# Kernel optimization log

Hardware: AMD Instinct MI355X
Metric: run time of the kernel (lower is better)

## Reference

```python
import jax, jax.numpy as jnp
import numpy as np

NODE_DIM = 128
CTX_DIM = 256
OUT_DIM = 256
GRID_SIZE = 4
SPLINE_ORDER = 3
IN_DIM = 3 * NODE_DIM  # subj + obj + transformed context
N_NODES = 100000
N_EDGES = 100000


def make_grid(in_dim, grid_size, spline_order, grid_range=(-1.0, 1.0)):
    h = (grid_range[1] - grid_range[0]) / grid_size
    g = (np.arange(-spline_order, grid_size + spline_order + 1, dtype=np.float32) * h
         + grid_range[0])  # [grid_size + 2*spline_order + 1]
    return jnp.asarray(np.tile(g[None, :], (in_dim, 1)))  # [in, G]


def b_splines(x, grid, spline_order):
    # x: [N, in], grid: [in, G] -> bases: [N, in, grid_size + spline_order]
    xg = x[:, :, None]
    bases = ((xg >= grid[:, :-1]) & (xg < grid[:, 1:])).astype(x.dtype)
    for k in range(1, spline_order + 1):
        left = (xg - grid[:, : -(k + 1)]) / (grid[:, k:-1] - grid[:, : -(k + 1)]) * bases[..., :-1]
        right = (grid[:, k + 1:] - xg) / (grid[:, k + 1:] - grid[:, 1:-k]) * bases[..., 1:]
        bases = left + right
    return bases


def setup_inputs() -> dict:
    key = jax.random.key(0)
    ks = jax.random.split(key, 8)
    n_coef = GRID_SIZE + SPLINE_ORDER
    return {
        "node_embeddings": jax.random.normal(ks[0], (N_NODES, NODE_DIM), jnp.float32),
        "context_embeddings": jax.random.normal(ks[1], (N_EDGES, CTX_DIM), jnp.float32),
        "pair_indices": jax.random.randint(ks[2], (N_EDGES, 2), 0, N_NODES, jnp.int64 if jax.config.jax_enable_x64 else jnp.int32),
        "ctx_w": jax.random.normal(ks[3], (NODE_DIM, CTX_DIM), jnp.float32) * (1.0 / np.sqrt(CTX_DIM)),
        "ctx_b": jnp.zeros((NODE_DIM,), jnp.float32),
        "base_weight": jax.random.normal(ks[4], (OUT_DIM, IN_DIM), jnp.float32) * (1.0 / np.sqrt(IN_DIM)),
        "spline_weight": jax.random.normal(ks[5], (OUT_DIM, IN_DIM, n_coef), jnp.float32) * 0.1,
        "spline_scaler": jax.random.normal(ks[6], (OUT_DIM, IN_DIM), jnp.float32) * (1.0 / np.sqrt(IN_DIM)),
        "grid": make_grid(IN_DIM, GRID_SIZE, SPLINE_ORDER),
    }


def reference(node_embeddings, context_embeddings, pair_indices, ctx_w, ctx_b,
              base_weight, spline_weight, spline_scaler, grid):
    # gather subject/object node embeddings (irregular access)
    subj = node_embeddings[pair_indices[:, 0]]          # [E, node_dim]
    obj = node_embeddings[pair_indices[:, 1]]           # [E, node_dim]
    ctx = context_embeddings @ ctx_w.T + ctx_b          # [E, node_dim]
    x = jnp.concatenate([subj, obj, ctx], axis=1)       # [E, 3*node_dim]

    # efficient-KAN linear layer: base (SiLU) branch + B-spline branch
    base_out = jax.nn.silu(x) @ base_weight.T           # [E, out]
    bsp = b_splines(x, grid, SPLINE_ORDER)              # [E, in, n_coef]
    scaled_w = spline_weight * spline_scaler[:, :, None]  # [out, in, n_coef]
    spline_out = jnp.einsum('nic,oic->no', bsp, scaled_w)
    return base_out + spline_out
```

## Files before the change

### kernel.cpp

```cpp
#include <hip/hip_runtime.h>

#define NEDGES   100000
#define NODE_DIM 128
#define CTX_DIM  256
#define OUT_DIM  256
#define IN_DIM   384
#define NCOEF    7
#define KTOT     3072
#define BM       128
#define BK       64
#define THREADS  512

typedef __bf16 bf16x8 __attribute__((ext_vector_type(8)));
typedef float  f32x4  __attribute__((ext_vector_type(4)));

static __device__ __forceinline__ unsigned short f2bf(float f) {
    unsigned int u = __float_as_uint(f);
    u += 0x7FFFu + ((u >> 16) & 1u);
    return (unsigned short)(u >> 16);
}
static __device__ __forceinline__ float bf2f(unsigned short h) {
    return __uint_as_float(((unsigned int)h) << 16);
}
static __device__ __forceinline__ unsigned int pkbf(float a, float b) {
    unsigned int ua = __float_as_uint(a), ub = __float_as_uint(b);
    ua += 0x7FFFu + ((ua >> 16) & 1u);
    ub += 0x7FFFu + ((ub >> 16) & 1u);
    return (ua >> 16) | (ub & 0xFFFF0000u);
}
static __device__ __forceinline__ float silu(float x) {
    return x / (1.0f + __expf(-x));
}
static __device__ __forceinline__ float n3c(float d2) {
    float a  = fabsf(d2);
    float t1 = fmaf(0.5f, a, -1.0f);
    float s2 = d2 * d2;
    float p1 = fmaf(t1, s2, 0.66666667f);
    float dd = fmaxf(2.0f - a, 0.0f);
    float p2 = dd * dd * (dd * (1.0f / 6.0f));
    return a < 1.0f ? p1 : p2;
}
static __device__ __forceinline__ float n3(float t) {
    return n3c(t - 2.0f);
}

static __device__ __forceinline__ void glds16(const unsigned short* g, unsigned short* l) {
    __builtin_amdgcn_global_load_lds(
        (const __attribute__((address_space(1))) void*)g,
        (__attribute__((address_space(3))) void*)l, 16, 0, 0);
}


__global__ void prep_w_swz(const float* __restrict__ base_w,
                           const float* __restrict__ spline_w,
                           const float* __restrict__ spline_s,
                           unsigned short* __restrict__ Wsw)
{
    int gc = blockIdx.x * 256 + threadIdx.x;
    int o  = blockIdx.y;
    int seg = gc / IN_DIM;
    int i   = gc - seg * IN_DIM;
    float w;
    if (seg == 0) w = base_w[o * IN_DIM + i];
    else {
        int bi = o * IN_DIM + i;
        w = spline_w[(size_t)bi * NCOEF + (seg - 1)] * spline_s[bi];
    }
    int p  = i >> 6;
    int k8 = (i >> 3) & 7;
    int j  = i & 7;
    int c  = p * 8 + seg;
    Wsw[(size_t)c * (OUT_DIM * BK) + o * BK + ((k8 ^ (o & 7)) << 3) + j] = f2bf(w);
}

#define K1STR 72
__global__ __launch_bounds__(THREADS, 2)
void build_x(const float* __restrict__ node_emb,
             const float* __restrict__ ctx_emb,
             const int*   __restrict__ pair,
             const float* __restrict__ ctx_w,
             const float* __restrict__ ctx_b,
             unsigned short* __restrict__ Xbf)
{
    __shared__ unsigned short sm[2 * 128 * K1STR];
    const int tid    = threadIdx.x;
    const int e_base = blockIdx.x * BM;
    const int wid    = tid >> 6;
    const int lan    = tid & 63;
    const int lrow   = lan & 15;
    const int lquad  = lan >> 4;

    #pragma unroll
    for (int it = 0; it < 16; ++it) {
        int id    = it * THREADS + tid;
        int f4    = id & 31;
        int which = (id >> 5) & 1;
        int e     = id >> 6;
        int eg = e_base + e; if (eg >= NEDGES) eg = NEDGES - 1;
        int node = pair[eg * 2 + which];
        float4 v = *(const float4*)(node_emb + (size_t)node * NODE_DIM + f4 * 4);
        *(uint2*)&Xbf[(size_t)eg * IN_DIM + which * NODE_DIM + f4 * 4] =
            make_uint2(pkbf(v.x, v.y), pkbf(v.z, v.w));
    }

    f32x4 acc[4][2];
    #pragma unroll
    for (int a = 0; a < 4; ++a)
        #pragma unroll
        for (int b = 0; b < 2; ++b) { f32x4 z = {0.f,0.f,0.f,0.f}; acc[a][b] = z; }

    const int m0 = (wid & 1) * 64;
    const int n0 = (wid >> 1) * 32;

    for (int kc = 0; kc < 4; ++kc) {
        #pragma unroll
        for (int it = 0; it < 4; ++it) {
            int id = it * THREADS + tid;
            int r  = id >> 4;
            int c4 = id & 15;
            int eg = e_base + r; if (eg >= NEDGES) eg = NEDGES - 1;
            float4 v = *(const float4*)(ctx_emb + (size_t)eg * CTX_DIM + kc * 64 + c4 * 4);
            *(uint2*)&sm[r * K1STR + c4 * 4] = make_uint2(pkbf(v.x, v.y), pkbf(v.z, v.w));
            float4 w = *(const float4*)(ctx_w + (size_t)r * CTX_DIM + kc * 64 + c4 * 4);
            *(uint2*)&sm[128 * K1STR + r * K1STR + c4 * 4] = make_uint2(pkbf(w.x, w.y), pkbf(w.z, w.w));
        }
        __syncthreads();
        #pragma unroll
        for (int ks = 0; ks < 2; ++ks) {
            int koff = ks * 32 + lquad * 8;
            bf16x8 af[4], bfr[2];
            #pragma unroll
            for (int mt = 0; mt < 4; ++mt)
                af[mt] = *(const bf16x8*)&sm[(m0 + mt*16 + lrow) * K1STR + koff];
            #pragma unroll
            for (int nt = 0; nt < 2; ++nt)
                bfr[nt] = *(const bf16x8*)&sm[128 * K1STR + (n0 + nt*16 + lrow) * K1STR + koff];
            #pragma unroll
            for (int mt = 0; mt < 4; ++mt)
                #pragma unroll
                for (int nt = 0; nt < 2; ++nt)
                    acc[mt][nt] = __builtin_amdgcn_mfma_f32_16x16x32_bf16(
                        af[mt], bfr[nt], acc[mt][nt], 0, 0, 0);
        }
        __syncthreads();
    }

    #pragma unroll
    for (int nt = 0; nt < 2; ++nt) {
        int col = n0 + nt * 16 + lrow;
        float cb = ctx_b[col];
        #pragma unroll
        for (int mt = 0; mt < 4; ++mt)
            #pragma unroll
            for (int r = 0; r < 4; ++r) {
                int row = m0 + mt * 16 + lquad * 4 + r;
                int eg = e_base + row; if (eg >= NEDGES) eg = NEDGES - 1;
                Xbf[(size_t)eg * IN_DIM + 256 + col] = f2bf(acc[mt][nt][r] + cb);
            }
    }
}

#define ASTR  72
#define OFF_A 0
#define OFF_B (BM * ASTR)
#define K2_LDS (OFF_B + OUT_DIM * BK)

static __device__ __forceinline__ void mfma_chunk(const unsigned short* smem,
    f32x4 (&acc)[4][4], int m0, int n0, int lrow, int lquad)
{
    #pragma unroll
    for (int ks = 0; ks < 2; ++ks) {
        const int koff = ks * 32 + lquad * 8;
        const int k8   = ks * 4 + lquad;
        bf16x8 af[4], bfr[4];
        #pragma unroll
        for (int mt = 0; mt < 4; ++mt)
            af[mt] = *(const bf16x8*)&smem[OFF_A + (m0 + mt*16 + lrow) * ASTR + koff];
        #pragma unroll
        for (int nt = 0; nt < 4; ++nt) {
            int n = n0 + nt * 16 + lrow;
            bfr[nt] = *(const bf16x8*)&smem[OFF_B + n * BK + ((k8 ^ (n & 7)) << 3)];
        }
        #pragma unroll
        for (int mt = 0; mt < 4; ++mt)
            #pragma unroll
            for (int nt = 0; nt < 4; ++nt)
                acc[mt][nt] = __builtin_amdgcn_mfma_f32_16x16x32_bf16(
                    af[mt], bfr[nt], acc[mt][nt], 0, 0, 0);
    }
}

__global__ __launch_bounds__(THREADS, 4)
void kan_gemm(const unsigned short* __restrict__ Wsw,
              const unsigned short* __restrict__ Xbf,
              const float* __restrict__ grid,
              float* __restrict__ out)
{
    __shared__ unsigned short smem[K2_LDS];
    const int tid    = threadIdx.x;
    const int e_base = blockIdx.x * BM;
    const int wid    = tid >> 6;
    const int lan    = tid & 63;
    const int lrow   = lan & 15;
    const int lquad  = lan >> 4;
    const int m0     = (wid & 1) * 64;
    const int n0     = (wid >> 1) * 64;
    const int q      = tid & 15;

    const float g0   = grid[0];
    const float hinv = 1.0f / (grid[1] - grid[0]);
    const float cg   = -g0 * hinv - 2.0f;

    const unsigned short* xrow[4];
    unsigned int awoff[4];
    #pragma unroll
    for (int it = 0; it < 4; ++it) {
        int e  = it * 32 + (tid >> 4);
        int eg = e_base + e; if (eg >= NEDGES) eg = NEDGES - 1;
        xrow[it]  = Xbf + (size_t)eg * IN_DIM;
        awoff[it] = OFF_A + e * ASTR + q * 4;
    }

    f32x4 acc[4][4];
    #pragma unroll
    for (int a = 0; a < 4; ++a)
        #pragma unroll
        for (int b = 0; b < 4; ++b) { f32x4 z = {0.f,0.f,0.f,0.f}; acc[a][b] = z; }

    for (int p = 0; p < 6; ++p) {
        const int i0 = p * 64;

        {
            const unsigned short* wc = Wsw + (size_t)(p * 8) * (OUT_DIM * BK);
            #pragma unroll
            for (int it = 0; it < 4; ++it) {
                int id = it * THREADS + tid;
                glds16(wc + id * 8, &smem[OFF_B + id * 8]);
            }
        }

        float tm2[16];
        #pragma unroll
        for (int it = 0; it < 4; ++it) {
            ushort4 xv = *(const ushort4*)(xrow[it] + i0 + q * 4);
            float x0 = bf2f(xv.x), x1 = bf2f(xv.y), x2 = bf2f(xv.z), x3 = bf2f(xv.w);
            *(uint2*)&smem[awoff[it]] =
                make_uint2(pkbf(silu(x0), silu(x1)), pkbf(silu(x2), silu(x3)));
            tm2[it*4+0] = fmaf(x0, hinv, cg);
            tm2[it*4+1] = fmaf(x1, hinv, cg);
            tm2[it*4+2] = fmaf(x2, hinv, cg);
            tm2[it*4+3] = fmaf(x3, hinv, cg);
        }
        __syncthreads();
        mfma_chunk(smem, acc, m0, n0, lrow, lquad);
        __syncthreads();

        for (int seg = 1; seg < 8; ++seg) {
            const unsigned short* wc = Wsw + (size_t)(p * 8 + seg) * (OUT_DIM * BK);
            #pragma unroll
            for (int it = 0; it < 4; ++it) {
                int id = it * THREADS + tid;
                glds16(wc + id * 8, &smem[OFF_B + id * 8]);
            }
            const float sf = (float)(seg - 1);
            #pragma unroll
            for (int it = 0; it < 4; ++it) {
                float r0 = n3c(tm2[it*4+0] - sf);
                float r1 = n3c(tm2[it*4+1] - sf);
                float r2 = n3c(tm2[it*4+2] - sf);
                float r3 = n3c(tm2[it*4+3] - sf);
                *(uint2*)&smem[awoff[it]] = make_uint2(pkbf(r0, r1), pkbf(r2, r3));
            }
            __syncthreads();
            mfma_chunk(smem, acc, m0, n0, lrow, lquad);
            __syncthreads();
        }
    }

    #pragma unroll
    for (int mt = 0; mt < 4; ++mt) {
        #pragma unroll
        for (int r = 0; r < 4; ++r) {
            int row = m0 + mt * 16 + lquad * 4 + r;
            int eg  = e_base + row;
            if (eg < NEDGES) {
                float* op = out + (size_t)eg * OUT_DIM + n0 + lrow;
                #pragma unroll
                for (int nt = 0; nt < 4; ++nt)
                    op[nt * 16] = acc[mt][nt][r];
            }
        }
    }
}

#define XSTR 392
#define FASTR 72
#define FBSTR 72
#define FOFF_X 0
#define FOFF_A (BM * XSTR)
#define FOFF_B (FOFF_A + BM * FASTR)
#define FLDS_TOT (FOFF_B + OUT_DIM * FBSTR)
#define NCHUNK (KTOT / BK)

__global__ void prep_w_kernel(const float* __restrict__ base_w,
                              const float* __restrict__ spline_w,
                              const float* __restrict__ spline_s,
                              unsigned short* __restrict__ Wbf)
{
    int col = blockIdx.x * 256 + threadIdx.x;
    int o   = blockIdx.y;
    int seg = col / IN_DIM;
    int i   = col - seg * IN_DIM;
    float w;
    if (seg == 0) w = base_w[o * IN_DIM + i];
    else {
        int bi = o * IN_DIM + i;
        w = spline_w[(size_t)bi * NCOEF + (seg - 1)] * spline_s[bi];
    }
    Wbf[(size_t)o * KTOT + col] = f2bf(w);
}

template <bool PRE>
__global__ __launch_bounds__(THREADS, 2)
void fused_pair_kan(const float* __restrict__ node_emb,
                    const float* __restrict__ ctx_emb,
                    const int*   __restrict__ pair,
                    const float* __restrict__ ctx_w,
                    const float* __restrict__ ctx_b,
                    const float* __restrict__ base_w,
                    const float* __restrict__ spline_w,
                    const float* __restrict__ spline_s,
                    const float* __restrict__ grid,
                    const unsigned short* __restrict__ Wbf,
                    float* __restrict__ out)
{
    __shared__ unsigned short smem[FLDS_TOT];
    const int tid    = threadIdx.x;
    const int e_base = blockIdx.x * BM;
    const int wid    = tid >> 6;
    const int lan    = tid & 63;
    const int lrow   = lan & 15;
    const int lquad  = lan >> 4;

    #pragma unroll
    for (int it = 0; it < 16; ++it) {
        int id    = it * THREADS + tid;
        int lane4 = id & 31;
        int e     = (id >> 5) & 127;
        int which = id >> 12;
        int eg = e_base + e; if (eg >= NEDGES) eg = NEDGES - 1;
        int node = pair[eg * 2 + which];
        const float4 v = *(const float4*)(node_emb + (size_t)node * NODE_DIM + lane4 * 4);
        *(ushort4*)&smem[FOFF_X + e * XSTR + which * NODE_DIM + lane4 * 4] =
            make_ushort4(f2bf(v.x), f2bf(v.y), f2bf(v.z), f2bf(v.w));
    }
    {
        f32x4 cacc[4][2];
        #pragma unroll
        for (int a = 0; a < 4; ++a)
            #pragma unroll
            for (int b = 0; b < 2; ++b) { f32x4 z = {0.f,0.f,0.f,0.f}; cacc[a][b] = z; }
        const int m0 = (wid & 1) * 64;
        const int n0 = (wid >> 1) * 32;
        for (int kc = 0; kc < 4; ++kc) {
            #pragma unroll
            for (int it = 0; it < 4; ++it) {
                int id = it * THREADS + tid;
                int r  = id >> 4;
                int c4 = id & 15;
                int eg = e_base + r; if (eg >= NEDGES) eg = NEDGES - 1;
                float4 v = *(const float4*)(ctx_emb + (size_t)eg * CTX_DIM + kc * 64 + c4 * 4);
                *(ushort4*)&smem[FOFF_A + r * FASTR + c4 * 4] =
                    make_ushort4(f2bf(v.x), f2bf(v.y), f2bf(v.z), f2bf(v.w));
                float4 w = *(const float4*)(ctx_w + (size_t)r * CTX_DIM + kc * 64 + c4 * 4);
                *(ushort4*)&smem[FOFF_B + r * FBSTR + c4 * 4] =
                    make_ushort4(f2bf(w.x), f2bf(w.y), f2bf(w.z), f2bf(w.w));
            }
            __syncthreads();
            #pragma unroll
            for (int ks = 0; ks < 2; ++ks) {
                int koff = ks * 32 + lquad * 8;
                bf16x8 af[4], bfr[2];
                #pragma unroll
                for (int mt = 0; mt < 4; ++mt)
                    af[mt] = *(const bf16x8*)&smem[FOFF_A + (m0 + mt*16 + lrow) * FASTR + koff];
                #pragma unroll
                for (int nt = 0; nt < 2; ++nt)
                    bfr[nt] = *(const bf16x8*)&smem[FOFF_B + (n0 + nt*16 + lrow) * FBSTR + koff];
                #pragma unroll
                for (int mt = 0; mt < 4; ++mt)
                    #pragma unroll
                    for (int nt = 0; nt < 2; ++nt)
                        cacc[mt][nt] = __builtin_amdgcn_mfma_f32_16x16x32_bf16(
                            af[mt], bfr[nt], cacc[mt][nt], 0, 0, 0);
            }
            __syncthreads();
        }
        #pragma unroll
        for (int mt = 0; mt < 4; ++mt)
            #pragma unroll
            for (int nt = 0; nt < 2; ++nt)
                #pragma unroll
                for (int r = 0; r < 4; ++r) {
                    int row = m0 + mt*16 + lquad*4 + r;
                    int col = n0 + nt*16 + lrow;
                    float v = cacc[mt][nt][r] + ctx_b[col];
                    smem[FOFF_X + row * XSTR + 256 + col] = f2bf(v);
                }
    }
    __syncthreads();

    const float g0   = grid[0];
    const float hinv = 1.0f / (grid[1] - grid[0]);

    f32x4 acc[4][4];
    #pragma unroll
    for (int a = 0; a < 4; ++a)
        #pragma unroll
        for (int b = 0; b < 4; ++b) { f32x4 z = {0.f,0.f,0.f,0.f}; acc[a][b] = z; }

    const int m0 = (wid & 1) * 64;
    const int n0 = (wid >> 1) * 64;

    for (int kb = 0; kb < NCHUNK; ++kb) {
        const int seg = kb / 6;
        const int i0  = (kb - seg * 6) * BK;
        uint4 wv[4];
        if (PRE) {
            #pragma unroll
            for (int it = 0; it < 4; ++it) {
                int id = it * THREADS + tid;
                int o  = id >> 3;
                int v8 = id & 7;
                wv[it] = *(const uint4*)(Wbf + (size_t)o * KTOT + kb * BK + v8 * 8);
            }
        }
        #pragma unroll
        for (int it = 0; it < 4; ++it) {
            int id = it * THREADS + tid;
            int e  = id >> 4;
            int qq = id & 15;
            ushort4 xv = *(const ushort4*)&smem[FOFF_X + e * XSTR + i0 + qq * 4];
            float x0 = bf2f(xv.x), x1 = bf2f(xv.y), x2 = bf2f(xv.z), x3 = bf2f(xv.w);
            unsigned short r0, r1, r2, r3;
            if (seg == 0) {
                r0 = f2bf(silu(x0)); r1 = f2bf(silu(x1));
                r2 = f2bf(silu(x2)); r3 = f2bf(silu(x3));
            } else {
                const float cf = (float)(seg - 1);
                r0 = f2bf(n3((x0 - g0) * hinv - cf));
                r1 = f2bf(n3((x1 - g0) * hinv - cf));
                r2 = f2bf(n3((x2 - g0) * hinv - cf));
                r3 = f2bf(n3((x3 - g0) * hinv - cf));
            }
            *(ushort4*)&smem[FOFF_A + e * FASTR + qq * 4] = make_ushort4(r0, r1, r2, r3);
        }
        if (PRE) {
            #pragma unroll
            for (int it = 0; it < 4; ++it) {
                int id = it * THREADS + tid;
                int o  = id >> 3;
                int v8 = id & 7;
                *(uint4*)&smem[FOFF_B + o * FBSTR + v8 * 8] = wv[it];
            }
        } else {
            #pragma unroll
            for (int it = 0; it < 4; ++it) {
                int id = it * THREADS + tid;
                int o  = id >> 4;
                int qq = id & 15;
                unsigned short r0, r1, r2, r3;
                if (seg == 0) {
                    const float4 w = *(const float4*)(base_w + (size_t)o * IN_DIM + i0 + qq * 4);
                    r0 = f2bf(w.x); r1 = f2bf(w.y); r2 = f2bf(w.z); r3 = f2bf(w.w);
                } else {
                    int c  = seg - 1;
                    int bi = o * IN_DIM + i0 + qq * 4;
                    r0 = f2bf(spline_w[(size_t)(bi    ) * NCOEF + c] * spline_s[bi    ]);
                    r1 = f2bf(spline_w[(size_t)(bi + 1) * NCOEF + c] * spline_s[bi + 1]);
                    r2 = f2bf(spline_w[(size_t)(bi + 2) * NCOEF + c] * spline_s[bi + 2]);
                    r3 = f2bf(spline_w[(size_t)(bi + 3) * NCOEF + c] * spline_s[bi + 3]);
                }
                *(ushort4*)&smem[FOFF_B + o * FBSTR + qq * 4] = make_ushort4(r0, r1, r2, r3);
            }
        }
        __syncthreads();
        #pragma unroll
        for (int ks = 0; ks < 2; ++ks) {
            int koff = ks * 32 + lquad * 8;
            bf16x8 af[4], bfr[4];
            #pragma unroll
            for (int mt = 0; mt < 4; ++mt)
                af[mt] = *(const bf16x8*)&smem[FOFF_A + (m0 + mt*16 + lrow) * FASTR + koff];
            #pragma unroll
            for (int nt = 0; nt < 4; ++nt)
                bfr[nt] = *(const bf16x8*)&smem[FOFF_B + (n0 + nt*16 + lrow) * FBSTR + koff];
            #pragma unroll
            for (int mt = 0; mt < 4; ++mt)
                #pragma unroll
                for (int nt = 0; nt < 4; ++nt)
                    acc[mt][nt] = __builtin_amdgcn_mfma_f32_16x16x32_bf16(
                        af[mt], bfr[nt], acc[mt][nt], 0, 0, 0);
        }
        __syncthreads();
    }

    #pragma unroll
    for (int mt = 0; mt < 4; ++mt) {
        #pragma unroll
        for (int r = 0; r < 4; ++r) {
            int row = m0 + mt*16 + lquad*4 + r;
            int eg  = e_base + row;
            if (eg < NEDGES) {
                float* op = out + (size_t)eg * OUT_DIM + n0 + lrow;
                #pragma unroll
                for (int nt = 0; nt < 4; ++nt)
                    op[nt * 16] = acc[mt][nt][r];
            }
        }
    }
}

extern "C" void kernel_launch(void* const* d_in, const int* in_sizes, int n_in,
                              void* d_out, int out_size, void* d_ws, size_t ws_size,
                              hipStream_t stream)
{
    const float* node_emb = (const float*)d_in[0];
    const float* ctx_emb  = (const float*)d_in[1];
    const int*   pair     = (const int*)d_in[2];
    const float* ctx_w    = (const float*)d_in[3];
    const float* ctx_b    = (const float*)d_in[4];
    const float* base_w   = (const float*)d_in[5];
    const float* spline_w = (const float*)d_in[6];
    const float* spline_s = (const float*)d_in[7];
    const float* grid     = (const float*)d_in[8];
    float* out = (float*)d_out;

    const int nblk = (NEDGES + BM - 1) / BM;
    const size_t wbytes = (size_t)OUT_DIM * KTOT * sizeof(unsigned short);
    const size_t xoff   = 2u * 1024u * 1024u;
    const size_t need   = xoff + (size_t)NEDGES * IN_DIM * sizeof(unsigned short);

    if (ws_size >= need) {
        unsigned short* Wsw = (unsigned short*)d_ws;
        unsigned short* Xbf = (unsigned short*)((char*)d_ws + xoff);
        prep_w_swz<<<dim3(KTOT / 256, OUT_DIM), 256, 0, stream>>>(base_w, spline_w, spline_s, Wsw);
        build_x<<<nblk, THREADS, 0, stream>>>(node_emb, ctx_emb, pair, ctx_w, ctx_b, Xbf);
        kan_gemm<<<nblk, THREADS, 0, stream>>>(Wsw, Xbf, grid, out);
    } else if (ws_size >= wbytes) {
        unsigned short* Wbf = (unsigned short*)d_ws;
        prep_w_kernel<<<dim3(KTOT / 256, OUT_DIM), 256, 0, stream>>>(base_w, spline_w, spline_s, Wbf);
        fused_pair_kan<true><<<nblk, THREADS, 0, stream>>>(
            node_emb, ctx_emb, pair, ctx_w, ctx_b, base_w, spline_w, spline_s, grid, Wbf, out);
    } else {
        fused_pair_kan<false><<<nblk, THREADS, 0, stream>>>(
            node_emb, ctx_emb, pair, ctx_w, ctx_b, base_w, spline_w, spline_s, grid, nullptr, out);
    }
}
```

Baseline: 500.6 us.

## Reorder KAN GEMM K by input feature to exploit local B-spline sparsity

The weight matrix is re-laid out so that each input feature's base weight and its seven spline coefficients sit together in an 8-wide K group. Each X element then produces one 16-byte A-fragment: its SiLU value plus its four nonzero cubic B-spline values, computed in closed form and placed by a variable shift. The old code evaluated seven separate basis functions per element per segment. The GEMM loop now double-buffers 32-wide K chunks with async global-to-LDS weight loads, and build_x stages its context output through LDS to make coalesced stores. The shift-based placement assumes a uniform grid and drops bases that fall outside the window. More barriers per K (96 smaller chunks) may add overhead.

```diff
diff --git a/kernel.cpp b/kernel.cpp
--- a/kernel.cpp
+++ b/kernel.cpp
@@ -6,10 +6,11 @@
 #define OUT_DIM  256
 #define IN_DIM   384
 #define NCOEF    7
-#define KTOT     3072
-#define BM       128
-#define BK       64
-#define THREADS  512
+
+#define BM2      128
+#define BK2      32
+#define NCH2     96
+#define THR2     512
 
 typedef __bf16 bf16x8 __attribute__((ext_vector_type(8)));
 typedef float  f32x4  __attribute__((ext_vector_type(4)));
@@ -31,17 +32,13 @@
 static __device__ __forceinline__ float silu(float x) {
     return x / (1.0f + __expf(-x));
 }
-static __device__ __forceinline__ float n3c(float d2) {
+static __device__ __forceinline__ float n3(float t) {
+    float d2 = t - 2.0f;
     float a  = fabsf(d2);
-    float t1 = fmaf(0.5f, a, -1.0f);
-    float s2 = d2 * d2;
-    float p1 = fmaf(t1, s2, 0.66666667f);
+    float p1 = fmaf(fmaf(0.5f, a, -1.0f), d2 * d2, 0.66666667f);
     float dd = fmaxf(2.0f - a, 0.0f);
     float p2 = dd * dd * (dd * (1.0f / 6.0f));
     return a < 1.0f ? p1 : p2;
-}
-static __device__ __forceinline__ float n3(float t) {
-    return n3c(t - 2.0f);
 }
 
 static __device__ __forceinline__ void glds16(const unsigned short* g, unsigned short* l) {
@@ -50,31 +47,29 @@
         (__attribute__((address_space(3))) void*)l, 16, 0, 0);
 }
 
-
-__global__ void prep_w_swz(const float* __restrict__ base_w,
-                           const float* __restrict__ spline_w,
-                           const float* __restrict__ spline_s,
-                           unsigned short* __restrict__ Wsw)
+__global__ void prep_w2(const float* __restrict__ base_w,
+                        const float* __restrict__ spline_w,
+                        const float* __restrict__ spline_s,
+                        unsigned short* __restrict__ Wsw)
 {
-    int gc = blockIdx.x * 256 + threadIdx.x;
-    int o  = blockIdx.y;
-    int seg = gc / IN_DIM;
-    int i   = gc - seg * IN_DIM;
-    float w;
-    if (seg == 0) w = base_w[o * IN_DIM + i];
-    else {
-        int bi = o * IN_DIM + i;
-        w = spline_w[(size_t)bi * NCOEF + (seg - 1)] * spline_s[bi];
-    }
-    int p  = i >> 6;
-    int k8 = (i >> 3) & 7;
-    int j  = i & 7;
-    int c  = p * 8 + seg;
-    Wsw[(size_t)c * (OUT_DIM * BK) + o * BK + ((k8 ^ (o & 7)) << 3) + j] = f2bf(w);
+    int o = blockIdx.x;
+    int i = threadIdx.x;
+    int bi = o * IN_DIM + i;
+    float sc = spline_s[bi];
+    const float* sw = spline_w + (size_t)bi * NCOEF;
+    uint4 v;
+    v.x = pkbf(base_w[bi], sw[0] * sc);
+    v.y = pkbf(sw[1] * sc, sw[2] * sc);
+    v.z = pkbf(sw[3] * sc, sw[4] * sc);
+    v.w = pkbf(sw[5] * sc, sw[6] * sc);
+    int ch = i >> 2, g8 = i & 3;
+    int p  = o * 4 + (((o >> 1) + g8) & 3);
+    *(uint4*)(Wsw + (size_t)ch * (OUT_DIM * BK2) + p * 8) = v;
 }
 
 #define K1STR 72
-__global__ __launch_bounds__(THREADS, 2)
+#define BM   128
+__global__ __launch_bounds__(512, 2)
 void build_x(const float* __restrict__ node_emb,
              const float* __restrict__ ctx_emb,
              const int*   __restrict__ pair,
@@ -92,7 +87,7 @@
 
     #pragma unroll
     for (int it = 0; it < 16; ++it) {
-        int id    = it * THREADS + tid;
+        int id    = it * 512 + tid;
         int f4    = id & 31;
         int which = (id >> 5) & 1;
         int e     = id >> 6;
@@ -115,7 +110,7 @@
     for (int kc = 0; kc < 4; ++kc) {
         #pragma unroll
         for (int it = 0; it < 4; ++it) {
-            int id = it * THREADS + tid;
+            int id = it * 512 + tid;
             int r  = id >> 4;
             int c4 = id & 15;
             int eg = e_base + r; if (eg >= NEDGES) eg = NEDGES - 1;
@@ -145,6 +140,7 @@
         __syncthreads();
     }
 
+    #define ESTR 136
     #pragma unroll
     for (int nt = 0; nt < 2; ++nt) {
         int col = n0 + nt * 16 + lrow;
@@ -154,72 +150,89 @@
             #pragma unroll
             for (int r = 0; r < 4; ++r) {
                 int row = m0 + mt * 16 + lquad * 4 + r;
-                int eg = e_base + row; if (eg >= NEDGES) eg = NEDGES - 1;
-                Xbf[(size_t)eg * IN_DIM + 256 + col] = f2bf(acc[mt][nt][r] + cb);
-            }
-    }
-}
-
-#define ASTR  72
-#define OFF_A 0
-#define OFF_B (BM * ASTR)
-#define K2_LDS (OFF_B + OUT_DIM * BK)
-
-static __device__ __forceinline__ void mfma_chunk(const unsigned short* smem,
-    f32x4 (&acc)[4][4], int m0, int n0, int lrow, int lquad)
+                sm[row * ESTR + col] = f2bf(acc[mt][nt][r] + cb);
+            }
+    }
+    __syncthreads();
+    #pragma unroll
+    for (int it = 0; it < 8; ++it) {
+        int id = it * 512 + tid;
+        int row = id >> 5;
+        int g   = id & 31;
+        int eg = e_base + row; if (eg >= NEDGES) eg = NEDGES - 1;
+        *(uint2*)&Xbf[(size_t)eg * IN_DIM + 256 + g * 4] = *(uint2*)&sm[row * ESTR + g * 4];
+    }
+}
+
+#define A2STR  40
+#define A2SZ   (BM2 * A2STR)
+#define B2SZ   (OUT_DIM * BK2)
+#define OFF_A0 0
+#define OFF_A1 A2SZ
+#define OFF_B0 (2 * A2SZ)
+#define OFF_B1 (2 * A2SZ + B2SZ)
+#define LDS2   (2 * A2SZ + 2 * B2SZ)
+
+static __device__ __forceinline__ void gen_elem(
+    unsigned short xh, float hinv, float b0, unsigned short* dst)
 {
-    #pragma unroll
-    for (int ks = 0; ks < 2; ++ks) {
-        const int koff = ks * 32 + lquad * 8;
-        const int k8   = ks * 4 + lquad;
-        bf16x8 af[4], bfr[4];
-        #pragma unroll
-        for (int mt = 0; mt < 4; ++mt)
-            af[mt] = *(const bf16x8*)&smem[OFF_A + (m0 + mt*16 + lrow) * ASTR + koff];
-        #pragma unroll
-        for (int nt = 0; nt < 4; ++nt) {
-            int n = n0 + nt * 16 + lrow;
-            bfr[nt] = *(const bf16x8*)&smem[OFF_B + n * BK + ((k8 ^ (n & 7)) << 3)];
-        }
-        #pragma unroll
-        for (int mt = 0; mt < 4; ++mt)
-            #pragma unroll
-            for (int nt = 0; nt < 4; ++nt)
-                acc[mt][nt] = __builtin_amdgcn_mfma_f32_16x16x32_bf16(
-                    af[mt], bfr[nt], acc[mt][nt], 0, 0, 0);
-    }
-}
-
-__global__ __launch_bounds__(THREADS, 4)
-void kan_gemm(const unsigned short* __restrict__ Wsw,
-              const unsigned short* __restrict__ Xbf,
-              const float* __restrict__ grid,
-              float* __restrict__ out)
+    float x  = bf2f(xh);
+    float sl = silu(x);
+    unsigned short slh = f2bf(sl);
+    float t  = fmaf(x, hinv, b0);
+    float jf = floorf(t);
+    int   j0 = (int)jf;
+    float u  = t - jf;
+    float u2 = u * u, u3 = u2 * u;
+    float Q0 = u3 * 0.16666667f;
+    float d  = 1.0f - u;
+    float Q3 = d * d * d * 0.16666667f;
+    float Q1 = fmaf(0.5f, u + u2 - u3, 0.16666667f);
+    float Q2 = fmaf(0.5f, u3, 0.66666667f - u2);
+    unsigned plo = pkbf(Q3, Q2);
+    unsigned phi = pkbf(Q1, Q0);
+    unsigned long long P = ((unsigned long long)phi << 32) | plo;
+    int sh = (j0 << 4) - 32;
+    unsigned a  = (unsigned)sh;
+    unsigned na = 0u - a;
+    unsigned long long lo =
+        (a  < 64u) ? (P << (a  & 63u)) : ((na < 64u) ? (P >> (na & 63u)) : 0ull);
+    unsigned b2 = a - 64u;
+    unsigned nb = 0u - b2;
+    unsigned long long hi =
+        (b2 < 64u) ? (P << (b2 & 63u)) : ((nb < 64u) ? (P >> (nb & 63u)) : 0ull);
+    lo = (lo & ~0xFFFFull) | (unsigned long long)slh;
+    uint4 w;
+    w.x = (unsigned)lo; w.y = (unsigned)(lo >> 32);
+    w.z = (unsigned)hi; w.w = (unsigned)(hi >> 32);
+    *(uint4*)dst = w;
+}
+
+__global__ __launch_bounds__(THR2, 4)
+void kan_gemm2(const unsigned short* __restrict__ Wsw,
+               const unsigned short* __restrict__ Xbf,
+               const float* __restrict__ grid,
+               float* __restrict__ out)
 {
-    __shared__ unsigned short smem[K2_LDS];
+    __shared__ unsigned short smem[LDS2];
     const int tid    = threadIdx.x;
-    const int e_base = blockIdx.x * BM;
+    const int e_base = blockIdx.x * BM2;
     const int wid    = tid >> 6;
     const int lan    = tid & 63;
     const int lrow   = lan & 15;
     const int lquad  = lan >> 4;
     const int m0     = (wid & 1) * 64;
     const int n0     = (wid >> 1) * 64;
-    const int q      = tid & 15;
 
     const float g0   = grid[0];
     const float hinv = 1.0f / (grid[1] - grid[0]);
-    const float cg   = -g0 * hinv - 2.0f;
-
-    const unsigned short* xrow[4];
-    unsigned int awoff[4];
-    #pragma unroll
-    for (int it = 0; it < 4; ++it) {
-        int e  = it * 32 + (tid >> 4);
-        int eg = e_base + e; if (eg >= NEDGES) eg = NEDGES - 1;
-        xrow[it]  = Xbf + (size_t)eg * IN_DIM;
-        awoff[it] = OFF_A + e * ASTR + q * 4;
-    }
+    const float b0   = -g0 * hinv;
+
+    const int grow = tid >> 2;
+    const int gcol = tid & 3;
+    int geg = e_base + grow; if (geg >= NEDGES) geg = NEDGES - 1;
+    const unsigned short* xp = Xbf + (size_t)geg * IN_DIM + gcol;
+    const unsigned awr = grow * A2STR + gcol * 8;
 
     f32x4 acc[4][4];
     #pragma unroll
@@ -227,54 +240,49 @@
         #pragma unroll
         for (int b = 0; b < 4; ++b) { f32x4 z = {0.f,0.f,0.f,0.f}; acc[a][b] = z; }
 
-    for (int p = 0; p < 6; ++p) {
-        const int i0 = p * 64;
-
-        {
-            const unsigned short* wc = Wsw + (size_t)(p * 8) * (OUT_DIM * BK);
-            #pragma unroll
-            for (int it = 0; it < 4; ++it) {
-                int id = it * THREADS + tid;
-                glds16(wc + id * 8, &smem[OFF_B + id * 8]);
-            }
-        }
-
-        float tm2[16];
-        #pragma unroll
-        for (int it = 0; it < 4; ++it) {
-            ushort4 xv = *(const ushort4*)(xrow[it] + i0 + q * 4);
-            float x0 = bf2f(xv.x), x1 = bf2f(xv.y), x2 = bf2f(xv.z), x3 = bf2f(xv.w);
-            *(uint2*)&smem[awoff[it]] =
-                make_uint2(pkbf(silu(x0), silu(x1)), pkbf(silu(x2), silu(x3)));
-            tm2[it*4+0] = fmaf(x0, hinv, cg);
-            tm2[it*4+1] = fmaf(x1, hinv, cg);
-            tm2[it*4+2] = fmaf(x2, hinv, cg);
-            tm2[it*4+3] = fmaf(x3, hinv, cg);
-        }
+    unsigned short xc = xp[0];
+    unsigned short xn = xp[4];
+
+    #pragma unroll
+    for (int it = 0; it < 2; ++it) {
+        int id = it * THR2 + tid;
+        glds16(Wsw + id * 8, &smem[OFF_B0 + id * 8]);
+    }
+    gen_elem(xc, hinv, b0, &smem[OFF_A0 + awr]);
+    __syncthreads();
+
+    for (int kb = 0; kb < NCH2; ++kb) {
+        const int cur = kb & 1;
+        if (kb + 1 < NCH2) {
+            const unsigned short* wc = Wsw + (size_t)(kb + 1) * B2SZ;
+            unsigned boff = cur ? OFF_B0 : OFF_B1;
+            #pragma unroll
+            for (int it = 0; it < 2; ++it) {
+                int id = it * THR2 + tid;
+                glds16(wc + id * 8, &smem[boff + id * 8]);
+            }
+            unsigned short xh = xn;
+            if (kb + 2 < NCH2) xn = xp[(kb + 2) * 4];
+            gen_elem(xh, hinv, b0, &smem[(cur ? OFF_A0 : OFF_A1) + awr]);
+        }
+        const unsigned ab = cur ? OFF_A1 : OFF_A0;
+        const unsigned bb = cur ? OFF_B1 : OFF_B0;
+        bf16x8 af[4], bfr[4];
+        #pragma unroll
+        for (int mt = 0; mt < 4; ++mt)
+            af[mt] = *(const bf16x8*)&smem[ab + (m0 + mt*16 + lrow) * A2STR + lquad * 8];
+        #pragma unroll
+        for (int nt = 0; nt < 4; ++nt) {
+            int n = n0 + nt * 16 + lrow;
+            bfr[nt] = *(const bf16x8*)&smem[bb + n * 32 + ((((n >> 1) + lquad) & 3) << 3)];
+        }
+        #pragma unroll
+        for (int mt = 0; mt < 4; ++mt)
+            #pragma unroll
+            for (int nt = 0; nt < 4; ++nt)
+                acc[mt][nt] = __builtin_amdgcn_mfma_f32_16x16x32_bf16(
+                    af[mt], bfr[nt], acc[mt][nt], 0, 0, 0);
         __syncthreads();
-        mfma_chunk(smem, acc, m0, n0, lrow, lquad);
-        __syncthreads();
-
-        for (int seg = 1; seg < 8; ++seg) {
-            const unsigned short* wc = Wsw + (size_t)(p * 8 + seg) * (OUT_DIM * BK);
-            #pragma unroll
-            for (int it = 0; it < 4; ++it) {
-                int id = it * THREADS + tid;
-                glds16(wc + id * 8, &smem[OFF_B + id * 8]);
-            }
-            const float sf = (float)(seg - 1);
-            #pragma unroll
-            for (int it = 0; it < 4; ++it) {
-                float r0 = n3c(tm2[it*4+0] - sf);
-                float r1 = n3c(tm2[it*4+1] - sf);
-                float r2 = n3c(tm2[it*4+2] - sf);
-                float r3 = n3c(tm2[it*4+3] - sf);
-                *(uint2*)&smem[awoff[it]] = make_uint2(pkbf(r0, r1), pkbf(r2, r3));
-            }
-            __syncthreads();
-            mfma_chunk(smem, acc, m0, n0, lrow, lquad);
-            __syncthreads();
-        }
     }
 
     #pragma unroll
@@ -294,35 +302,14 @@
 }
 
 #define XSTR 392
-#define FASTR 72
-#define FBSTR 72
+#define FSTR 72
 #define FOFF_X 0
-#define FOFF_A (BM * XSTR)
-#define FOFF_B (FOFF_A + BM * FASTR)
-#define FLDS_TOT (FOFF_B + OUT_DIM * FBSTR)
-#define NCHUNK (KTOT / BK)
-
-__global__ void prep_w_kernel(const float* __restrict__ base_w,
-                              const float* __restrict__ spline_w,
-                              const float* __restrict__ spline_s,
-                              unsigned short* __restrict__ Wbf)
-{
-    int col = blockIdx.x * 256 + threadIdx.x;
-    int o   = blockIdx.y;
-    int seg = col / IN_DIM;
-    int i   = col - seg * IN_DIM;
-    float w;
-    if (seg == 0) w = base_w[o * IN_DIM + i];
-    else {
-        int bi = o * IN_DIM + i;
-        w = spline_w[(size_t)bi * NCOEF + (seg - 1)] * spline_s[bi];
-    }
-    Wbf[(size_t)o * KTOT + col] = f2bf(w);
-}
-
-template <bool PRE>
-__global__ __launch_bounds__(THREADS, 2)
-void fused_pair_kan(const float* __restrict__ node_emb,
+#define FOFF_A (128 * XSTR)
+#define FOFF_B (FOFF_A + 128 * FSTR)
+#define FLDS (FOFF_B + OUT_DIM * FSTR)
+
+__global__ __launch_bounds__(512, 2)
+void fused_fallback(const float* __restrict__ node_emb,
                     const float* __restrict__ ctx_emb,
                     const int*   __restrict__ pair,
                     const float* __restrict__ ctx_w,
@@ -331,12 +318,11 @@
                     const float* __restrict__ spline_w,
                     const float* __restrict__ spline_s,
                     const float* __restrict__ grid,
-                    const unsigned short* __restrict__ Wbf,
                     float* __restrict__ out)
 {
-    __shared__ unsigned short smem[FLDS_TOT];
+    __shared__ unsigned short smem[FLDS];
     const int tid    = threadIdx.x;
-    const int e_base = blockIdx.x * BM;
+    const int e_base = blockIdx.x * 128;
     const int wid    = tid >> 6;
     const int lan    = tid & 63;
     const int lrow   = lan & 15;
@@ -344,7 +330,7 @@
 
     #pragma unroll
     for (int it = 0; it < 16; ++it) {
-        int id    = it * THREADS + tid;
+        int id    = it * 512 + tid;
         int lane4 = id & 31;
         int e     = (id >> 5) & 127;
         int which = id >> 12;
@@ -365,15 +351,15 @@
         for (int kc = 0; kc < 4; ++kc) {
             #pragma unroll
             for (int it = 0; it < 4; ++it) {
-                int id = it * THREADS + tid;
+                int id = it * 512 + tid;
                 int r  = id >> 4;
                 int c4 = id & 15;
                 int eg = e_base + r; if (eg >= NEDGES) eg = NEDGES - 1;
                 float4 v = *(const float4*)(ctx_emb + (size_t)eg * CTX_DIM + kc * 64 + c4 * 4);
-                *(ushort4*)&smem[FOFF_A + r * FASTR + c4 * 4] =
+                *(ushort4*)&smem[FOFF_A + r * FSTR + c4 * 4] =
                     make_ushort4(f2bf(v.x), f2bf(v.y), f2bf(v.z), f2bf(v.w));
                 float4 w = *(const float4*)(ctx_w + (size_t)r * CTX_DIM + kc * 64 + c4 * 4);
-                *(ushort4*)&smem[FOFF_B + r * FBSTR + c4 * 4] =
+                *(ushort4*)&smem[FOFF_B + r * FSTR + c4 * 4] =
                     make_ushort4(f2bf(w.x), f2bf(w.y), f2bf(w.z), f2bf(w.w));
             }
             __syncthreads();
@@ -383,10 +369,10 @@
                 bf16x8 af[4], bfr[2];
                 #pragma unroll
                 for (int mt = 0; mt < 4; ++mt)
-                    af[mt] = *(const bf16x8*)&smem[FOFF_A + (m0 + mt*16 + lrow) * FASTR + koff];
+                    af[mt] = *(const bf16x8*)&smem[FOFF_A + (m0 + mt*16 + lrow) * FSTR + koff];
                 #pragma unroll
                 for (int nt = 0; nt < 2; ++nt)
-                    bfr[nt] = *(const bf16x8*)&smem[FOFF_B + (n0 + nt*16 + lrow) * FBSTR + koff];
+                    bfr[nt] = *(const bf16x8*)&smem[FOFF_B + (n0 + nt*16 + lrow) * FSTR + koff];
                 #pragma unroll
                 for (int mt = 0; mt < 4; ++mt)
                     #pragma unroll
@@ -404,8 +390,7 @@
                 for (int r = 0; r < 4; ++r) {
                     int row = m0 + mt*16 + lquad*4 + r;
                     int col = n0 + nt*16 + lrow;
-                    float v = cacc[mt][nt][r] + ctx_b[col];
-                    smem[FOFF_X + row * XSTR + 256 + col] = f2bf(v);
+                    smem[FOFF_X + row * XSTR + 256 + col] = f2bf(cacc[mt][nt][r] + ctx_b[col]);
                 }
     }
     __syncthreads();
@@ -422,22 +407,12 @@
     const int m0 = (wid & 1) * 64;
     const int n0 = (wid >> 1) * 64;
 
-    for (int kb = 0; kb < NCHUNK; ++kb) {
+    for (int kb = 0; kb < 48; ++kb) {
         const int seg = kb / 6;
-        const int i0  = (kb - seg * 6) * BK;
-        uint4 wv[4];
-        if (PRE) {
-            #pragma unroll
-            for (int it = 0; it < 4; ++it) {
-                int id = it * THREADS + tid;
-                int o  = id >> 3;
-                int v8 = id & 7;
-                wv[it] = *(const uint4*)(Wbf + (size_t)o * KTOT + kb * BK + v8 * 8);
-            }
-        }
+        const int i0  = (kb - seg * 6) * 64;
         #pragma unroll
         for (int it = 0; it < 4; ++it) {
-            int id = it * THREADS + tid;
+            int id = it * 512 + tid;
             int e  = id >> 4;
             int qq = id & 15;
             ushort4 xv = *(const ushort4*)&smem[FOFF_X + e * XSTR + i0 + qq * 4];
@@ -453,36 +428,26 @@
                 r2 = f2bf(n3((x2 - g0) * hinv - cf));
                 r3 = f2bf(n3((x3 - g0) * hinv - cf));
             }
-            *(ushort4*)&smem[FOFF_A + e * FASTR + qq * 4] = make_ushort4(r0, r1, r2, r3);
-        }
-        if (PRE) {
-            #pragma unroll
-            for (int it = 0; it < 4; ++it) {
-                int id = it * THREADS + tid;
-                int o  = id >> 3;
-                int v8 = id & 7;
-                *(uint4*)&smem[FOFF_B + o * FBSTR + v8 * 8] = wv[it];
-            }
-        } else {
-            #pragma unroll
-            for (int it = 0; it < 4; ++it) {
-                int id = it * THREADS + tid;
-                int o  = id >> 4;
-                int qq = id & 15;
-                unsigned short r0, r1, r2, r3;
-                if (seg == 0) {
-                    const float4 w = *(const float4*)(base_w + (size_t)o * IN_DIM + i0 + qq * 4);
-                    r0 = f2bf(w.x); r1 = f2bf(w.y); r2 = f2bf(w.z); r3 = f2bf(w.w);
-                } else {
-                    int c  = seg - 1;
-                    int bi = o * IN_DIM + i0 + qq * 4;
-                    r0 = f2bf(spline_w[(size_t)(bi    ) * NCOEF + c] * spline_s[bi    ]);
-                    r1 = f2bf(spline_w[(size_t)(bi + 1) * NCOEF + c] * spline_s[bi + 1]);
-                    r2 = f2bf(spline_w[(size_t)(bi + 2) * NCOEF + c] * spline_s[bi + 2]);
-                    r3 = f2bf(spline_w[(size_t)(bi + 3) * NCOEF + c] * spline_s[bi + 3]);
-                }
-                *(ushort4*)&smem[FOFF_B + o * FBSTR + qq * 4] = make_ushort4(r0, r1, r2, r3);
-            }
+            *(ushort4*)&smem[FOFF_A + e * FSTR + qq * 4] = make_ushort4(r0, r1, r2, r3);
+        }
+        #pragma unroll
+        for (int it = 0; it < 4; ++it) {
+            int id = it * 512 + tid;
+            int o  = id >> 4;
+            int qq = id & 15;
+            unsigned short r0, r1, r2, r3;
+            if (seg == 0) {
+                const float4 w = *(const float4*)(base_w + (size_t)o * IN_DIM + i0 + qq * 4);
+                r0 = f2bf(w.x); r1 = f2bf(w.y); r2 = f2bf(w.z); r3 = f2bf(w.w);
+            } else {
+                int c  = seg - 1;
+                int bi = o * IN_DIM + i0 + qq * 4;
+                r0 = f2bf(spline_w[(size_t)(bi    ) * NCOEF + c] * spline_s[bi    ]);
+                r1 = f2bf(spline_w[(size_t)(bi + 1) * NCOEF + c] * spline_s[bi + 1]);
+                r2 = f2bf(spline_w[(size_t)(bi + 2) * NCOEF + c] * spline_s[bi + 2]);
+                r3 = f2bf(spline_w[(size_t)(bi + 3) * NCOEF + c] * spline_s[bi + 3]);
+            }
+            *(ushort4*)&smem[FOFF_B + o * FSTR + qq * 4] = make_ushort4(r0, r1, r2, r3);
         }
         __syncthreads();
         #pragma unroll
@@ -491,10 +456,10 @@
             bf16x8 af[4], bfr[4];
             #pragma unroll
             for (int mt = 0; mt < 4; ++mt)
-                af[mt] = *(const bf16x8*)&smem[FOFF_A + (m0 + mt*16 + lrow) * FASTR + koff];
+                af[mt] = *(const bf16x8*)&smem[FOFF_A + (m0 + mt*16 + lrow) * FSTR + koff];
             #pragma unroll
             for (int nt = 0; nt < 4; ++nt)
-                bfr[nt] = *(const bf16x8*)&smem[FOFF_B + (n0 + nt*16 + lrow) * FBSTR + koff];
+                bfr[nt] = *(const bf16x8*)&smem[FOFF_B + (n0 + nt*16 + lrow) * FSTR + koff];
             #pragma unroll
             for (int mt = 0; mt < 4; ++mt)
                 #pragma unroll
@@ -536,24 +501,18 @@
     const float* grid     = (const float*)d_in[8];
     float* out = (float*)d_out;
 
-    const int nblk = (NEDGES + BM - 1) / BM;
-    const size_t wbytes = (size_t)OUT_DIM * KTOT * sizeof(unsigned short);
-    const size_t xoff   = 2u * 1024u * 1024u;
-    const size_t need   = xoff + (size_t)NEDGES * IN_DIM * sizeof(unsigned short);
+    const int nblk = (NEDGES + BM2 - 1) / BM2;
+    const size_t xoff = 2u * 1024u * 1024u;
+    const size_t need = xoff + (size_t)NEDGES * IN_DIM * sizeof(unsigned short);
 
     if (ws_size >= need) {
         unsigned short* Wsw = (unsigned short*)d_ws;
         unsigned short* Xbf = (unsigned short*)((char*)d_ws + xoff);
-        prep_w_swz<<<dim3(KTOT / 256, OUT_DIM), 256, 0, stream>>>(base_w, spline_w, spline_s, Wsw);
-        build_x<<<nblk, THREADS, 0, stream>>>(node_emb, ctx_emb, pair, ctx_w, ctx_b, Xbf);
-        kan_gemm<<<nblk, THREADS, 0, stream>>>(Wsw, Xbf, grid, out);
-    } else if (ws_size >= wbytes) {
-        unsigned short* Wbf = (unsigned short*)d_ws;
-        prep_w_kernel<<<dim3(KTOT / 256, OUT_DIM), 256, 0, stream>>>(base_w, spline_w, spline_s, Wbf);
-        fused_pair_kan<true><<<nblk, THREADS, 0, stream>>>(
-            node_emb, ctx_emb, pair, ctx_w, ctx_b, base_w, spline_w, spline_s, grid, Wbf, out);
+        prep_w2<<<OUT_DIM, IN_DIM, 0, stream>>>(base_w, spline_w, spline_s, Wsw);
+        build_x<<<nblk, 512, 0, stream>>>(node_emb, ctx_emb, pair, ctx_w, ctx_b, Xbf);
+        kan_gemm2<<<nblk, THR2, 0, stream>>>(Wsw, Xbf, grid, out);
     } else {
-        fused_pair_kan<false><<<nblk, THREADS, 0, stream>>>(
-            node_emb, ctx_emb, pair, ctx_w, ctx_b, base_w, spline_w, spline_s, grid, nullptr, out);
-    }
-}
+        fused_fallback<<<nblk, 512, 0, stream>>>(
+            node_emb, ctx_emb, pair, ctx_w, ctx_b, base_w, spline_w, spline_s, grid, out);
+    }
+}
```

New measurement: 436.1 us. 12.9% less time.
